# Kernel optimization log

Hardware: AMD Instinct MI355X
Metric: run time of the kernel (lower is better)

The kernel has to match this reference:

```python
import jax, jax.numpy as jnp
import numpy as np

B, C, H, W = 8, 512, 48, 48
DK = C // 8            # query/key dim
L = max(H, W)          # rel_pos_length == H == W
R = 2 * L - 1          # num relative shifts
N = H * W
EPS = 1e-5


def setup_inputs() -> dict:
    key = jax.random.key(0)
    ks = jax.random.split(key, 20)
    d = {
        "x": jax.random.normal(ks[0], (B, C, H, W), jnp.float32),
        "Wq": jax.random.normal(ks[1], (DK, C), jnp.float32) * 0.02,
        "bq": jnp.zeros((DK,), jnp.float32),
        "q_scale": jnp.ones((DK,), jnp.float32),
        "q_bias": jnp.zeros((DK,), jnp.float32),
        "Wk": jax.random.normal(ks[2], (DK, C), jnp.float32) * 0.02,
        "bk": jnp.zeros((DK,), jnp.float32),
        "k_scale": jnp.ones((DK,), jnp.float32),
        "k_bias": jnp.zeros((DK,), jnp.float32),
        "Wv": jax.random.normal(ks[3], (C, C), jnp.float32) * 0.02,
        "bv": jnp.zeros((C,), jnp.float32),
        "v_scale": jnp.ones((C,), jnp.float32),
        "v_bias": jnp.zeros((C,), jnp.float32),
        "rel_rows": jax.random.normal(ks[4], (R, DK), jnp.float32),
        "rel_columns": jax.random.normal(ks[5], (R, DK), jnp.float32),
        "bnr_scale": jnp.ones((C,), jnp.float32),
        "bnr_bias": jnp.zeros((C,), jnp.float32),
        "bnc_scale": jnp.ones((C,), jnp.float32),
        "bnc_bias": jnp.zeros((C,), jnp.float32),
        # gamma is a learned scalar (init 0 in torch; nonzero here so output != x)
        "gamma": jax.random.normal(ks[6], (1,), jnp.float32) * 0.1,
    }
    return d


def _bn(y, scale, bias):
    # train-mode BatchNorm2d: batch stats over (B,H,W), biased variance
    m = jnp.mean(y, axis=(0, 2, 3))
    v = jnp.mean((y - m[None, :, None, None]) ** 2, axis=(0, 2, 3))
    yn = (y - m[None, :, None, None]) * jax.lax.rsqrt(v + EPS)[None, :, None, None]
    return yn * scale[None, :, None, None] + bias[None, :, None, None]


def _conv_bn_relu(x, Wc, bc, scale, bias):
    y = jnp.einsum('bchw,oc->bohw', x, Wc) + bc[None, :, None, None]  # 1x1 conv
    return jax.nn.relu(_bn(y, scale, bias))


def _rel_P(l, rel_table):
    # compute_reindexing_tensor reduces to a one-hot over shift (i - x) since
    # |i-x| <= L always holds when L == l; Ih @ rel_table == gather by shift.
    x = jnp.arange(l)[:, None]
    i = jnp.arange(l)[None, :]
    idx = i - x + (L - 1)                 # (l, l) in [0, 2L-2]
    return rel_table[idx]                 # (l, l, DK)


def reference(x, Wq, bq, q_scale, q_bias, Wk, bk, k_scale, k_bias,
              Wv, bv, v_scale, v_bias, rel_rows, rel_columns,
              bnr_scale, bnr_bias, bnc_scale, bnc_bias, gamma):
    q = _conv_bn_relu(x, Wq, bq, q_scale, q_bias).reshape(B, DK, N)   # proj_query^T
    k = _conv_bn_relu(x, Wk, bk, k_scale, k_bias).reshape(B, DK, N)
    v = _conv_bn_relu(x, Wv, bv, v_scale, v_bias).reshape(B, C, N)

    energy = jnp.einsum('bdn,bdm->bnm', q, k)        # (B,N,N) = Q^T K (unscaled)
    attention = jax.nn.softmax(energy, axis=-1)
    out = jnp.einsum('bcj,bij->bci', v, attention)   # V A^T
    attn_mask = out.reshape(B, C, H, W)

    # relative position terms: Eh = V (Ph Q^T), Ew = V (Pw Q^T)
    Ph = _rel_P(H, rel_rows).reshape(N, DK)          # (N,DK) since H==W
    Mh = jnp.einsum('nd,bdm->bnm', Ph, q)
    Eh = jnp.einsum('bcn,bnm->bcm', v, Mh).reshape(B, C, H, W)
    Eh = _bn(Eh, bnr_scale, bnr_bias)

    Pw = _rel_P(W, rel_columns).reshape(N, DK)
    Mw = jnp.einsum('nd,bdm->bnm', Pw, q)
    Ew = jnp.einsum('bcn,bnm->bcm', v, Mw).reshape(B, C, H, W)
    Ew = _bn(Ew, bnc_scale, bnc_bias)

    attn_mask = attn_mask + Eh + Ew
    return gamma[0] * attn_mask + x
```

## Files before the change

kernel.cpp:

```cpp
#include <hip/hip_runtime.h>
#include <math.h>

#define BB   8
#define CIN  512
#define NSP  2304
#define OCH  640
#define LL   48

typedef __attribute__((ext_vector_type(8))) short bf16x8;
typedef __attribute__((ext_vector_type(8))) unsigned short u16x8;
typedef __attribute__((ext_vector_type(4))) float f32x4;

__device__ inline unsigned short f2bf(float f) {
  unsigned int u = __float_as_uint(f);
  unsigned int r = (u + 0x7fffu + ((u >> 16) & 1u)) >> 16;
  return (unsigned short)r;
}
__device__ inline float bf2f(unsigned short h) {
  return __uint_as_float(((unsigned int)h) << 16);
}


#define STAGE128x64(GP, LD, LDSN)                                              \
  {                                                                            \
    const unsigned short* gsrc_ = (GP);                                        \
    _Pragma("unroll") for (int cc_ = 0; cc_ < 4; cc_++) {                      \
      int base_ = w * 2048 + cc_ * 512;                                        \
      int row_ = w * 32 + cc_ * 8 + rsub;                                      \
      __builtin_amdgcn_global_load_lds(                                        \
          (const __attribute__((address_space(1))) void*)(gsrc_ +              \
              (size_t)row_ * (LD) + scolb),                                    \
          (__attribute__((address_space(3))) void*)&(LDSN)[base_], 16, 0, 0);  \
    }                                                                          \
  }

#define STAGE8(GPA, LDA, LA, GPB, LDB, LB)                                     \
  {                                                                            \
    if (w < 4) {                                                               \
      const unsigned short* gsrc_ = (GPA);                                     \
      _Pragma("unroll") for (int cc_ = 0; cc_ < 4; cc_++) {                    \
        int base_ = w * 2048 + cc_ * 512;                                      \
        int row_ = w * 32 + cc_ * 8 + rsub;                                    \
        __builtin_amdgcn_global_load_lds(                                      \
            (const __attribute__((address_space(1))) void*)(gsrc_ +            \
                (size_t)row_ * (LDA) + scolb),                                 \
            (__attribute__((address_space(3))) void*)&(LA)[base_], 16, 0, 0);  \
      }                                                                        \
    } else {                                                                   \
      const unsigned short* gsrc_ = (GPB);                                     \
      int w2_ = w - 4;                                                         \
      _Pragma("unroll") for (int cc_ = 0; cc_ < 4; cc_++) {                    \
        int base_ = w2_ * 2048 + cc_ * 512;                                    \
        int row_ = w2_ * 32 + cc_ * 8 + rsub;                                  \
        __builtin_amdgcn_global_load_lds(                                      \
            (const __attribute__((address_space(1))) void*)(gsrc_ +            \
                (size_t)row_ * (LDB) + scolb),                                 \
            (__attribute__((address_space(3))) void*)&(LB)[base_], 16, 0, 0);  \
      }                                                                        \
    }                                                                          \
  }

#define MFMA_STEP(APTR, BPTR)                                                  \
  _Pragma("unroll") for (int kk_ = 0; kk_ < 2; kk_++) {                        \
    bf16x8 af_[4], bf_[4];                                                     \
    int kcol_ = (((kk_ * 4 + (lane >> 4)) ^ (lane & 7)) * 8);                  \
    _Pragma("unroll") for (int m_ = 0; m_ < 4; m_++)                           \
      af_[m_] = *(const bf16x8*)&(APTR)[(wr * 64 + m_ * 16 + (lane & 15)) * 64 + kcol_]; \
    _Pragma("unroll") for (int n_ = 0; n_ < 4; n_++)                           \
      bf_[n_] = *(const bf16x8*)&(BPTR)[(wc * 64 + n_ * 16 + (lane & 15)) * 64 + kcol_]; \
    _Pragma("unroll") for (int m_ = 0; m_ < 4; m_++)                           \
      _Pragma("unroll") for (int n_ = 0; n_ < 4; n_++)                         \
        acc[m_][n_] = __builtin_amdgcn_mfma_f32_16x16x32_bf16(                 \
            af_[m_], bf_[n_], acc[m_][n_], 0, 0, 0);                           \
  }

#define MFMA_STEP8(APTR, BPTR)                                                 \
  _Pragma("unroll") for (int kk_ = 0; kk_ < 2; kk_++) {                        \
    bf16x8 af_[4], bf_[2];                                                     \
    int kcol_ = (((kk_ * 4 + (lane >> 4)) ^ (lane & 7)) * 8);                  \
    _Pragma("unroll") for (int m_ = 0; m_ < 4; m_++)                           \
      af_[m_] = *(const bf16x8*)&(APTR)[(wr * 64 + m_ * 16 + (lane & 15)) * 64 + kcol_]; \
    _Pragma("unroll") for (int n_ = 0; n_ < 2; n_++)                           \
      bf_[n_] = *(const bf16x8*)&(BPTR)[(wc * 32 + n_ * 16 + (lane & 15)) * 64 + kcol_]; \
    _Pragma("unroll") for (int m_ = 0; m_ < 4; m_++)                           \
      _Pragma("unroll") for (int n_ = 0; n_ < 2; n_++)                         \
        acc[m_][n_] = __builtin_amdgcn_mfma_f32_16x16x32_bf16(                 \
            af_[m_], bf_[n_], acc[m_][n_], 0, 0, 0);                           \
  }

#define MFMA_PROLOG()                                                          \
  const int tid = threadIdx.x;                                                 \
  const int lane = tid & 63;                                                   \
  const int w = tid >> 6;                                                      \
  const int wr = w >> 1, wc = w & 1;                                           \
  const int rsub = lane >> 3;                                                  \
  const int scolb = ((lane & 7) ^ rsub) * 8;                                   \
  f32x4 acc[4][4] = {};                                                        \
  (void)scolb; (void)rsub; (void)wr; (void)wc;

__global__ __launch_bounds__(256) void prep_all(
    const float* __restrict__ Wq, const float* __restrict__ bq,
    const float* __restrict__ Wk, const float* __restrict__ bk,
    const float* __restrict__ Wv, const float* __restrict__ bv,
    const float* __restrict__ rel_rows, const float* __restrict__ rel_cols,
    unsigned short* __restrict__ Wstb, float* __restrict__ bst,
    unsigned short* __restrict__ Pcatb) {
  int idx = blockIdx.x * 256 + threadIdx.x;
  if (idx < OCH * CIN) {
    int row = idx >> 9;
    float val;
    if (row < 64)       val = Wq[idx];
    else if (row < 128) val = Wk[idx - (64 << 9)];
    else                val = Wv[idx - (128 << 9)];
    Wstb[idx] = f2bf(val);
    if (idx < OCH) {
      float bval;
      if (idx < 64)       bval = bq[idx];
      else if (idx < 128) bval = bk[idx - 64];
      else                bval = bv[idx - 128];
      bst[idx] = bval;
    }
  } else {
    int p = idx - OCH * CIN;
    int dd = p / NSP;
    int n = p - dd * NSP;
    int xr = n / LL;
    int ic = n - xr * LL;
    int shift = ic - xr + (LL - 1);
    float val = (dd < 64) ? rel_rows[shift * 64 + dd]
                          : rel_cols[shift * 64 + (dd - 64)];
    Pcatb[p] = f2bf(val);
  }
}

__global__ __launch_bounds__(256) void transpose_x(
    const float* __restrict__ x, unsigned short* __restrict__ xTb) {
  __shared__ float t[64][65];
  const int n0 = blockIdx.x * 64;
  const int c0 = blockIdx.y * 64;
  const int b = blockIdx.z;
  const int j = threadIdx.x & 63;
  const int g = threadIdx.x >> 6;
  const float* xp = x + (size_t)b * CIN * NSP;
#pragma unroll
  for (int i = 0; i < 16; i++) {
    int cl = g * 16 + i;
    t[cl][j] = xp[(size_t)(c0 + cl) * NSP + n0 + j];
  }
  __syncthreads();
  unsigned short* op = xTb + (size_t)b * NSP * CIN;
#pragma unroll
  for (int i = 0; i < 16; i++) {
    int nl = g * 16 + i;
    op[(size_t)(n0 + nl) * CIN + c0 + j] = f2bf(t[j][nl]);
  }
}

__global__ __launch_bounds__(256) void proj_mfma(
    const unsigned short* __restrict__ Wstb, const float* __restrict__ bst,
    const unsigned short* __restrict__ xTb, unsigned short* __restrict__ y16,
    float* __restrict__ part1, float* __restrict__ part2) {
  __shared__ unsigned short As[2][8192];
  __shared__ unsigned short Bs[2][8192];
  int sw = ((blockIdx.x & 7) * 90) + (blockIdx.x >> 3);
  const int rb = sw % 5;
  const int nb = (sw / 5) % 18;
  const int b = sw / 90;
  const int r0 = rb * 128;
  const int n0 = nb * 128;
  MFMA_PROLOG();
  const unsigned short* A = Wstb + (size_t)r0 * CIN;
  const unsigned short* B = xTb + (size_t)b * NSP * CIN + (size_t)n0 * CIN;

  STAGE128x64(A, CIN, As[0]);
  STAGE128x64(B, CIN, Bs[0]);
  asm volatile("s_waitcnt vmcnt(0)" ::: "memory");
  __builtin_amdgcn_sched_barrier(0);
  __builtin_amdgcn_s_barrier();

  int cur = 0;
  for (int t = 0; t < 8; ++t) {
    if (t + 1 < 8) {
      STAGE128x64(A + (t + 1) * 64, CIN, As[cur ^ 1]);
      STAGE128x64(B + (t + 1) * 64, CIN, Bs[cur ^ 1]);
    }
    __builtin_amdgcn_s_setprio(1);
    MFMA_STEP(As[cur], Bs[cur]);
    __builtin_amdgcn_s_setprio(0);
    asm volatile("s_waitcnt vmcnt(0)" ::: "memory");
    __builtin_amdgcn_sched_barrier(0);
    __builtin_amdgcn_s_barrier();
    cur ^= 1;
  }

  float* sp = (float*)&As[0][0];
#pragma unroll
  for (int m = 0; m < 4; m++) {
#pragma unroll
    for (int r = 0; r < 4; r++) {
      int rl = wr * 64 + m * 16 + (lane >> 4) * 4 + r;
      int row = r0 + rl;
      float bias = bst[row];
      float s1 = 0.f, s2 = 0.f;
#pragma unroll
      for (int n = 0; n < 4; n++) {
        float yv = acc[m][n][r] + bias;
        s1 += yv;
        s2 += yv * yv;
        y16[((size_t)b * OCH + row) * NSP + n0 + wc * 64 + n * 16 + (lane & 15)] = f2bf(yv);
      }
#pragma unroll
      for (int off = 1; off < 16; off <<= 1) {
        s1 += __shfl_xor(s1, off);
        s2 += __shfl_xor(s2, off);
      }
      if ((lane & 15) == 0) {
        sp[rl * 2 + wc] = s1;
        sp[256 + rl * 2 + wc] = s2;
      }
    }
  }
  __syncthreads();
  if (tid < 128) {
    size_t pbase = ((size_t)b * 18 + nb) * OCH + r0 + tid;
    part1[pbase] = sp[tid * 2] + sp[tid * 2 + 1];
    part2[pbase] = sp[256 + tid * 2] + sp[256 + tid * 2 + 1];
  }
}

__global__ __launch_bounds__(256) void bn_finalize(
    const float* __restrict__ part1, const float* __restrict__ part2,
    const float* __restrict__ qs_, const float* __restrict__ qb_,
    const float* __restrict__ ks_, const float* __restrict__ kb_,
    const float* __restrict__ vs_, const float* __restrict__ vb_,
    float* __restrict__ chanA, float* __restrict__ chanB) {
  const int ch = blockIdx.x;
  const int tid = threadIdx.x;
  float s1 = 0.f, s2 = 0.f;
  for (int t = tid; t < 144; t += 256) {
    s1 += part1[(size_t)t * OCH + ch];
    s2 += part2[(size_t)t * OCH + ch];
  }
  __shared__ float sb[8];
#pragma unroll
  for (int off = 32; off > 0; off >>= 1) {
    s1 += __shfl_down(s1, off);
    s2 += __shfl_down(s2, off);
  }
  int lane = tid & 63, wid = tid >> 6;
  if (lane == 0) { sb[wid] = s1; sb[4 + wid] = s2; }
  __syncthreads();
  if (tid == 0) {
    float ts  = sb[0] + sb[1] + sb[2] + sb[3];
    float ts2 = sb[4] + sb[5] + sb[6] + sb[7];
    const float inv = 1.f / (float)(BB * NSP);
    float mean = ts * inv;
    float var  = ts2 * inv - mean * mean;
    float scale, bias;
    if (ch < 64)       { scale = qs_[ch];       bias = qb_[ch]; }
    else if (ch < 128) { scale = ks_[ch - 64];  bias = kb_[ch - 64]; }
    else               { scale = vs_[ch - 128]; bias = vb_[ch - 128]; }
    float a = scale * rsqrtf(var + 1e-5f);
    chanA[ch] = a;
    chanB[ch] = bias - mean * a;
  }
}

__global__ __launch_bounds__(256) void bn_post(
    unsigned short* __restrict__ y16, const float* __restrict__ chanA,
    const float* __restrict__ chanB, unsigned short* __restrict__ qTb,
    unsigned short* __restrict__ kTb) {
  __shared__ unsigned short qk[128][64];
  const int n0 = blockIdx.x * 64;
  const int b = blockIdx.y;
  const int tid = threadIdx.x;
#pragma unroll
  for (int k = 0; k < 20; k++) {
    int v = tid + k * 256;
    int ch = v >> 3;
    int n8 = (v & 7) * 8;
    size_t off = ((size_t)b * OCH + ch) * NSP + n0 + n8;
    float a = chanA[ch], bo = chanB[ch];
    ushort4 u0 = *(ushort4*)&y16[off];
    ushort4 u1 = *(ushort4*)&y16[off + 4];
    ushort4 o0, o1;
    o0.x = f2bf(fmaxf(0.f, a * bf2f(u0.x) + bo));
    o0.y = f2bf(fmaxf(0.f, a * bf2f(u0.y) + bo));
    o0.z = f2bf(fmaxf(0.f, a * bf2f(u0.z) + bo));
    o0.w = f2bf(fmaxf(0.f, a * bf2f(u0.w) + bo));
    o1.x = f2bf(fmaxf(0.f, a * bf2f(u1.x) + bo));
    o1.y = f2bf(fmaxf(0.f, a * bf2f(u1.y) + bo));
    o1.z = f2bf(fmaxf(0.f, a * bf2f(u1.z) + bo));
    o1.w = f2bf(fmaxf(0.f, a * bf2f(u1.w) + bo));
    *(ushort4*)&y16[off] = o0;
    *(ushort4*)&y16[off + 4] = o1;
    if (ch < 128) {
      *(ushort4*)&qk[ch][n8] = o0;
      *(ushort4*)&qk[ch][n8 + 4] = o1;
    }
  }
  __syncthreads();
#pragma unroll
  for (int it = 0; it < 4; it++) {
    int combo = (tid >> 6) + it * 4;
    int plane = combo >> 3;
    int dg = combo & 7;
    int nl = tid & 63;
    unsigned short tmp[8];
#pragma unroll
    for (int d = 0; d < 8; d++) tmp[d] = qk[plane * 64 + dg * 8 + d][nl];
    unsigned short* out = (plane == 0) ? qTb : kTb;
    *(u16x8*)&out[((size_t)b * NSP + n0 + nl) * 64 + dg * 8] = *(u16x8*)tmp;
  }
}

__global__ __launch_bounds__(256) void qsum_kernel(
    const unsigned short* __restrict__ y16, float* __restrict__ qs) {
  int bd = blockIdx.x;
  int b = bd >> 6, d = bd & 63;
  const ushort4* p = (const ushort4*)(y16 + ((size_t)b * OCH + d) * NSP);
  float s = 0.f;
  for (int t = threadIdx.x; t < NSP / 4; t += 256) {
    ushort4 u = p[t];
    s += bf2f(u.x) + bf2f(u.y) + bf2f(u.z) + bf2f(u.w);
  }
  __shared__ float sb[4];
#pragma unroll
  for (int off = 32; off > 0; off >>= 1) s += __shfl_down(s, off);
  int lane = threadIdx.x & 63, wid = threadIdx.x >> 6;
  if (lane == 0) sb[wid] = s;
  __syncthreads();
  if (threadIdx.x == 0) qs[bd] = sb[0] + sb[1] + sb[2] + sb[3];
}

__global__ __launch_bounds__(256) void gq_mfma(
    const unsigned short* __restrict__ y16, float* __restrict__ Gqp) {
  __shared__ float wlds[4 * 4096];
  const int bx = blockIdx.x;
  const int b = bx >> 2, kc = bx & 3;
  const int tid = threadIdx.x;
  const int lane = tid & 63;
  const int w = tid >> 6;
  const unsigned short* q = y16 + (size_t)b * OCH * NSP;
  f32x4 acc[4][4] = {};
  for (int k0 = kc * 576 + w * 32; k0 < (kc + 1) * 576; k0 += 128) {
    bf16x8 fr[4];
#pragma unroll
    for (int f = 0; f < 4; f++) {
      int row = f * 16 + (lane & 15);
      fr[f] = *(const bf16x8*)&q[(size_t)row * NSP + k0 + (lane >> 4) * 8];
    }
#pragma unroll
    for (int fm = 0; fm < 4; fm++)
#pragma unroll
      for (int fn = 0; fn < 4; fn++)
        acc[fm][fn] = __builtin_amdgcn_mfma_f32_16x16x32_bf16(
            fr[fm], fr[fn], acc[fm][fn], 0, 0, 0);
  }
#pragma unroll
  for (int fm = 0; fm < 4; fm++)
#pragma unroll
    for (int fn = 0; fn < 4; fn++)
#pragma unroll
      for (int r = 0; r < 4; r++) {
        int d = fm * 16 + (lane >> 4) * 4 + r;
        int e = fn * 16 + (lane & 15);
        wlds[w * 4096 + d * 64 + e] = acc[fm][fn][r];
      }
  __syncthreads();
  for (int t = tid; t < 4096; t += 256)
    Gqp[(size_t)bx * 4096 + t] =
        wlds[t] + wlds[4096 + t] + wlds[8192 + t] + wlds[12288 + t];
}

__global__ __launch_bounds__(256) void energy_mfma(
    const unsigned short* __restrict__ qTb, const unsigned short* __restrict__ kTb,
    unsigned short* __restrict__ Pp, float* __restrict__ Ppart) {
  __shared__ unsigned short As[8192];
  __shared__ unsigned short Bs[8192];
  int sw = ((blockIdx.x & 7) * 324) + (blockIdx.x >> 3);
  const int jb = sw % 18;
  const int ib = (sw / 18) % 18;
  const int b = sw / 324;
  const int i0 = ib * 128;
  const int j0 = jb * 128;
  MFMA_PROLOG();
  STAGE128x64(qTb + ((size_t)b * NSP + i0) * 64, 64, As);
  STAGE128x64(kTb + ((size_t)b * NSP + j0) * 64, 64, Bs);
  __syncthreads();
  MFMA_STEP(As, Bs);
  __syncthreads();
  float* sp = (float*)As;
  unsigned short* pp = Pp + (size_t)b * NSP * NSP;
#pragma unroll
  for (int m = 0; m < 4; m++) {
#pragma unroll
    for (int r = 0; r < 4; r++) {
      int rl = wr * 64 + m * 16 + (lane >> 4) * 4 + r;
      int i = i0 + rl;
      float s1 = 0.f;
#pragma unroll
      for (int n = 0; n < 4; n++) {
        int j = j0 + wc * 64 + n * 16 + (lane & 15);
        unsigned short h = f2bf(__expf(acc[m][n][r]));
        pp[(size_t)i * NSP + j] = h;
        s1 += bf2f(h);
      }
#pragma unroll
      for (int off = 1; off < 16; off <<= 1) s1 += __shfl_xor(s1, off);
      if ((lane & 15) == 0) sp[rl * 2 + wc] = s1;
    }
  }
  __syncthreads();
  if (tid < 128)
    Ppart[((size_t)b * 18 + jb) * NSP + i0 + tid] = sp[tid * 2] + sp[tid * 2 + 1];
}

__global__ __launch_bounds__(256) void up_mfma(
    const unsigned short* __restrict__ y16, const unsigned short* __restrict__ Pcatb,
    float* __restrict__ Upart) {
  __shared__ unsigned short As[2][8192];
  __shared__ unsigned short Bs[2][8192];
  int sw = ((blockIdx.x & 7) * 24) + (blockIdx.x >> 3);
  const int cb = sw % 4;
  const int kc = (sw / 4) % 6;
  const int b = sw / 24;
  const int c0 = cb * 128;
  MFMA_PROLOG();
  const unsigned short* A = y16 + ((size_t)b * OCH + 128 + c0) * NSP + kc * 384;
  const unsigned short* B = Pcatb + kc * 384;

  STAGE128x64(A, NSP, As[0]);
  STAGE128x64(B, NSP, Bs[0]);
  asm volatile("s_waitcnt vmcnt(0)" ::: "memory");
  __builtin_amdgcn_sched_barrier(0);
  __builtin_amdgcn_s_barrier();

  int cur = 0;
  for (int t = 0; t < 6; ++t) {
    if (t + 1 < 6) {
      STAGE128x64(A + (t + 1) * 64, NSP, As[cur ^ 1]);
      STAGE128x64(B + (t + 1) * 64, NSP, Bs[cur ^ 1]);
    }
    __builtin_amdgcn_s_setprio(1);
    MFMA_STEP(As[cur], Bs[cur]);
    __builtin_amdgcn_s_setprio(0);
    asm volatile("s_waitcnt vmcnt(0)" ::: "memory");
    __builtin_amdgcn_sched_barrier(0);
    __builtin_amdgcn_s_barrier();
    cur ^= 1;
  }

  float* up = Upart + ((size_t)kc * BB + b) * CIN * 128 + (size_t)c0 * 128;
#pragma unroll
  for (int m = 0; m < 4; m++)
#pragma unroll
    for (int r = 0; r < 4; r++) {
      int rl = wr * 64 + m * 16 + (lane >> 4) * 4 + r;
#pragma unroll
      for (int n = 0; n < 4; n++) {
        int col = wc * 64 + n * 16 + (lane & 15);
        up[(size_t)rl * 128 + col] = acc[m][n][r];
      }
    }
}

__global__ __launch_bounds__(256) void rel_finalize(
    const float* __restrict__ Upart, const float* __restrict__ Gqp,
    const float* __restrict__ qs,
    const float* __restrict__ bnr_s, const float* __restrict__ bnr_b,
    const float* __restrict__ bnc_s, const float* __restrict__ bnc_b,
    float* __restrict__ offc, unsigned short* __restrict__ Ucb) {
  const int c = blockIdx.x;
  const int tid = threadIdx.x;
  __shared__ float U[8][128];
  __shared__ float ghw[2];
  for (int t = tid; t < 1024; t += 256) {
    int b = t >> 7, dd = t & 127;
    float s = 0.f;
#pragma unroll
    for (int kc = 0; kc < 6; kc++)
      s += Upart[(((size_t)kc * BB + b) * CIN + c) * 128 + dd];
    U[b][dd] = s;
  }
  __syncthreads();
  if (tid < 64) {
    const int d = tid;
    float s1h = 0.f, s2h = 0.f, s1w = 0.f, s2w = 0.f;
    for (int b = 0; b < BB; b++) {
      float uh = U[b][d], uw = U[b][64 + d];
      float th = 0.f, tw = 0.f;
#pragma unroll
      for (int kc = 0; kc < 4; kc++) {
        const float* G = Gqp + ((size_t)(b * 4 + kc)) * 4096 + d * 64;
        for (int e = 0; e < 64; e++) {
          float g = G[e];
          th += g * U[b][e];
          tw += g * U[b][64 + e];
        }
      }
      float qsd = qs[b * 64 + d];
      s1h += uh * qsd;
      s2h += uh * th;
      s1w += uw * qsd;
      s2w += uw * tw;
    }
#pragma unroll
    for (int off = 32; off > 0; off >>= 1) {
      s1h += __shfl_down(s1h, off);
      s2h += __shfl_down(s2h, off);
      s1w += __shfl_down(s1w, off);
      s2w += __shfl_down(s2w, off);
    }
    if (d == 0) {
      const float inv = 1.f / (float)(BB * NSP);
      float mh = s1h * inv, vh = s2h * inv - mh * mh;
      float mw = s1w * inv, vw = s2w * inv - mw * mw;
      float gch = bnr_s[c] * rsqrtf(vh + 1e-5f);
      float gcw = bnc_s[c] * rsqrtf(vw + 1e-5f);
      ghw[0] = gch;
      ghw[1] = gcw;
      offc[c] = (bnr_b[c] - mh * gch) + (bnc_b[c] - mw * gcw);
    }
  }
  __syncthreads();
  for (int t = tid; t < 512; t += 256) {
    int b = t >> 6, d = t & 63;
    Ucb[((size_t)b * CIN + c) * 64 + d] =
        f2bf(U[b][d] * ghw[0] + U[b][64 + d] * ghw[1]);
  }
}

__global__ __launch_bounds__(512) void attn_fused_gemm(
    const unsigned short* __restrict__ y16,
    const unsigned short* __restrict__ Pp,
    const float* __restrict__ Ppart,
    const unsigned short* __restrict__ Ucb,
    const unsigned short* __restrict__ qTb,
    const float* __restrict__ offc,
    const float* __restrict__ gammap,
    const float* __restrict__ x,
    float* __restrict__ dst) {
  __shared__ unsigned short As[2][8192];
  __shared__ unsigned short Bs[2][8192];
  __shared__ float rzl[128];
  int sw = ((blockIdx.x & 7) * 72) + (blockIdx.x >> 3);
  const int cb = sw % 4;
  const int ib = (sw / 4) % 18;
  const int b = sw / 72;
  const int c0 = cb * 128;
  const int i0 = ib * 128;
  const int tid = threadIdx.x;
  const int lane = tid & 63;
  const int w = tid >> 6;
  const int wr = w >> 2, wc = w & 3;
  const int rsub = lane >> 3;
  const int scolb = ((lane & 7) ^ rsub) * 8;
  f32x4 acc[4][2] = {};

  const unsigned short* A = y16 + ((size_t)b * OCH + 128 + c0) * NSP;
  const unsigned short* B = Pp + (size_t)b * NSP * NSP + (size_t)i0 * NSP;
  const unsigned short* A2 = Ucb + (size_t)b * CIN * 64 + (size_t)c0 * 64;
  const unsigned short* B2 = qTb + (size_t)b * NSP * 64 + (size_t)i0 * 64;

  STAGE8(A, NSP, As[0], B, NSP, Bs[0]);
  if (tid < 128) {
    float s = 0.f;
#pragma unroll
    for (int jb = 0; jb < 18; jb++)
      s += Ppart[((size_t)b * 18 + jb) * NSP + i0 + tid];
    rzl[tid] = 1.f / s;
  }
  asm volatile("s_waitcnt vmcnt(0)" ::: "memory");
  __builtin_amdgcn_sched_barrier(0);
  __builtin_amdgcn_s_barrier();

  int cur = 0;
  for (int tt = 0; tt < 37; ++tt) {
    if (tt + 1 < 36) {
      STAGE8(A + (tt + 1) * 64, NSP, As[cur ^ 1], B + (tt + 1) * 64, NSP, Bs[cur ^ 1]);
    } else if (tt + 1 == 36) {
      STAGE8(A2, 64, As[cur ^ 1], B2, 64, Bs[cur ^ 1]);
    }
    if (tt == 36) {
#pragma unroll
      for (int n = 0; n < 2; n++) {
        float rz = rzl[wc * 32 + n * 16 + (lane & 15)];
#pragma unroll
        for (int m = 0; m < 4; m++)
#pragma unroll
          for (int r = 0; r < 4; r++) acc[m][n][r] *= rz;
      }
    }
    __builtin_amdgcn_s_setprio(1);
    MFMA_STEP8(As[cur], Bs[cur]);
    __builtin_amdgcn_s_setprio(0);
    asm volatile("s_waitcnt vmcnt(0)" ::: "memory");
    __builtin_amdgcn_sched_barrier(0);
    __builtin_amdgcn_s_barrier();
    cur ^= 1;
  }

  const float gmm = gammap[0];
  const float* xp = x + (size_t)b * CIN * NSP;
  float* dp = dst + (size_t)b * CIN * NSP;
#pragma unroll
  for (int m = 0; m < 4; m++) {
#pragma unroll
    for (int r = 0; r < 4; r++) {
      int c = c0 + wr * 64 + m * 16 + (lane >> 4) * 4 + r;
      float off = offc[c];
#pragma unroll
      for (int n = 0; n < 2; n++) {
        int i = i0 + wc * 32 + n * 16 + (lane & 15);
        size_t o = (size_t)c * NSP + i;
        dp[o] = gmm * (acc[m][n][r] + off) + xp[o];
      }
    }
  }
}

extern "C" void kernel_launch(void* const* d_in, const int* in_sizes, int n_in,
                              void* d_out, int out_size, void* d_ws, size_t ws_size,
                              hipStream_t stream) {
  const float* x        = (const float*)d_in[0];
  const float* Wq       = (const float*)d_in[1];
  const float* bq       = (const float*)d_in[2];
  const float* q_scale  = (const float*)d_in[3];
  const float* q_bias   = (const float*)d_in[4];
  const float* Wk       = (const float*)d_in[5];
  const float* bk       = (const float*)d_in[6];
  const float* k_scale  = (const float*)d_in[7];
  const float* k_bias   = (const float*)d_in[8];
  const float* Wv       = (const float*)d_in[9];
  const float* bv       = (const float*)d_in[10];
  const float* v_scale  = (const float*)d_in[11];
  const float* v_bias   = (const float*)d_in[12];
  const float* rel_rows = (const float*)d_in[13];
  const float* rel_cols = (const float*)d_in[14];
  const float* bnr_s    = (const float*)d_in[15];
  const float* bnr_b    = (const float*)d_in[16];
  const float* bnc_s    = (const float*)d_in[17];
  const float* bnc_b    = (const float*)d_in[18];
  const float* gamma    = (const float*)d_in[19];
  float* dst = (float*)d_out;

  float* ws = (float*)d_ws;
  size_t o = 0;
  unsigned short* Wstb = (unsigned short*)(ws + o); o += (size_t)OCH * CIN / 2;
  float* bst    = ws + o; o += 1024;
  float* chanA  = ws + o; o += 1024;
  float* chanB  = ws + o; o += 1024;
  unsigned short* Pcatb = (unsigned short*)(ws + o); o += (size_t)128 * NSP / 2;
  unsigned short* y16 = (unsigned short*)(ws + o); o += (size_t)BB * OCH * NSP / 2;
  unsigned short* xTb = (unsigned short*)(ws + o); o += (size_t)BB * NSP * CIN / 2;
  unsigned short* Pp  = (unsigned short*)(ws + o); o += (size_t)BB * NSP * NSP / 2;
  float* Ppart  = ws + o; o += (size_t)BB * 18 * NSP;
  float* Upart  = ws + o; o += (size_t)6 * BB * CIN * 128;
  float* Gqp    = ws + o; o += (size_t)32 * 4096;
  float* part1  = ws + o; o += (size_t)BB * 18 * OCH;
  float* part2  = ws + o; o += (size_t)BB * 18 * OCH;
  float* qs     = ws + o; o += 1024;
  float* offc   = ws + o; o += 1024;
  unsigned short* qTb = (unsigned short*)(ws + o); o += (size_t)BB * NSP * 64 / 2;
  unsigned short* kTb = (unsigned short*)(ws + o); o += (size_t)BB * NSP * 64 / 2;
  unsigned short* Ucb = (unsigned short*)(ws + o); o += (size_t)BB * CIN * 64 / 2;

  prep_all<<<(OCH * CIN + 128 * NSP) / 256, 256, 0, stream>>>(
      Wq, bq, Wk, bk, Wv, bv, rel_rows, rel_cols, Wstb, bst, Pcatb);
  transpose_x<<<dim3(NSP / 64, CIN / 64, BB), 256, 0, stream>>>(x, xTb);

  proj_mfma<<<720, 256, 0, stream>>>(Wstb, bst, xTb, y16, part1, part2);
  bn_finalize<<<OCH, 256, 0, stream>>>(part1, part2, q_scale, q_bias, k_scale,
                                       k_bias, v_scale, v_bias, chanA, chanB);
  bn_post<<<dim3(36, BB), 256, 0, stream>>>(y16, chanA, chanB, qTb, kTb);
  qsum_kernel<<<BB * 64, 256, 0, stream>>>(y16, qs);
  gq_mfma<<<32, 256, 0, stream>>>(y16, Gqp);

  energy_mfma<<<2592, 256, 0, stream>>>(qTb, kTb, Pp, Ppart);

  up_mfma<<<192, 256, 0, stream>>>(y16, Pcatb, Upart);
  rel_finalize<<<CIN, 256, 0, stream>>>(Upart, Gqp, qs, bnr_s, bnr_b,
                                        bnc_s, bnc_b, offc, Ucb);

  attn_fused_gemm<<<576, 512, 0, stream>>>(y16, Pp, Ppart, Ucb, qTb, offc, gamma, x, dst);
}
```

Measured before the change: 240.2 us.

## Deepen attention GEMM pipeline, coalesce energy stores, fold qsum into gq kernel

The attention GEMM moves from double to quad-buffered LDS staging with a prefetch distance of two and partial vmcnt waits, so global loads overlap more MFMA work. The energy kernel now stages its exp tile in LDS and writes it out as 16-byte vectors instead of scattered 2-byte stores. The separate qsum kernel is removed and its row sums are computed as per-chunk partials inside gq_mfma, then summed in rel_finalize. Doubling LDS in the attention kernel (about 128 KB) may reduce occupancy.

```diff
diff --git a/kernel.cpp b/kernel.cpp
--- a/kernel.cpp
+++ b/kernel.cpp
@@ -6,6 +6,9 @@
 #define NSP  2304
 #define OCH  640
 #define LL   48
+
+#define AS1 __attribute__((address_space(1)))
+#define AS3 __attribute__((address_space(3)))
 
 typedef __attribute__((ext_vector_type(8))) short bf16x8;
 typedef __attribute__((ext_vector_type(8))) unsigned short u16x8;
@@ -28,9 +31,8 @@
       int base_ = w * 2048 + cc_ * 512;                                        \
       int row_ = w * 32 + cc_ * 8 + rsub;                                      \
       __builtin_amdgcn_global_load_lds(                                        \
-          (const __attribute__((address_space(1))) void*)(gsrc_ +              \
-              (size_t)row_ * (LD) + scolb),                                    \
-          (__attribute__((address_space(3))) void*)&(LDSN)[base_], 16, 0, 0);  \
+          (const AS1 void*)(gsrc_ + (size_t)row_ * (LD) + scolb),              \
+          (AS3 void*)&(LDSN)[base_], 16, 0, 0);                                \
     }                                                                          \
   }
 
@@ -42,9 +44,8 @@
         int base_ = w * 2048 + cc_ * 512;                                      \
         int row_ = w * 32 + cc_ * 8 + rsub;                                    \
         __builtin_amdgcn_global_load_lds(                                      \
-            (const __attribute__((address_space(1))) void*)(gsrc_ +            \
-                (size_t)row_ * (LDA) + scolb),                                 \
-            (__attribute__((address_space(3))) void*)&(LA)[base_], 16, 0, 0);  \
+            (const AS1 void*)(gsrc_ + (size_t)row_ * (LDA) + scolb),           \
+            (AS3 void*)&(LA)[base_], 16, 0, 0);                                \
       }                                                                        \
     } else {                                                                   \
       const unsigned short* gsrc_ = (GPB);                                     \
@@ -53,9 +54,8 @@
         int base_ = w2_ * 2048 + cc_ * 512;                                    \
         int row_ = w2_ * 32 + cc_ * 8 + rsub;                                  \
         __builtin_amdgcn_global_load_lds(                                      \
-            (const __attribute__((address_space(1))) void*)(gsrc_ +            \
-                (size_t)row_ * (LDB) + scolb),                                 \
-            (__attribute__((address_space(3))) void*)&(LB)[base_], 16, 0, 0);  \
+            (const AS1 void*)(gsrc_ + (size_t)row_ * (LDB) + scolb),           \
+            (AS3 void*)&(LB)[base_], 16, 0, 0);                                \
       }                                                                        \
     }                                                                          \
   }
@@ -314,27 +314,9 @@
   }
 }
 
-__global__ __launch_bounds__(256) void qsum_kernel(
-    const unsigned short* __restrict__ y16, float* __restrict__ qs) {
-  int bd = blockIdx.x;
-  int b = bd >> 6, d = bd & 63;
-  const ushort4* p = (const ushort4*)(y16 + ((size_t)b * OCH + d) * NSP);
-  float s = 0.f;
-  for (int t = threadIdx.x; t < NSP / 4; t += 256) {
-    ushort4 u = p[t];
-    s += bf2f(u.x) + bf2f(u.y) + bf2f(u.z) + bf2f(u.w);
-  }
-  __shared__ float sb[4];
-#pragma unroll
-  for (int off = 32; off > 0; off >>= 1) s += __shfl_down(s, off);
-  int lane = threadIdx.x & 63, wid = threadIdx.x >> 6;
-  if (lane == 0) sb[wid] = s;
-  __syncthreads();
-  if (threadIdx.x == 0) qs[bd] = sb[0] + sb[1] + sb[2] + sb[3];
-}
-
 __global__ __launch_bounds__(256) void gq_mfma(
-    const unsigned short* __restrict__ y16, float* __restrict__ Gqp) {
+    const unsigned short* __restrict__ y16, float* __restrict__ Gqp,
+    float* __restrict__ qsp) {
   __shared__ float wlds[4 * 4096];
   const int bx = blockIdx.x;
   const int b = bx >> 2, kc = bx & 3;
@@ -367,6 +349,17 @@
         int e = fn * 16 + (lane & 15);
         wlds[w * 4096 + d * 64 + e] = acc[fm][fn][r];
       }
+  {
+    float s = 0.f;
+    const unsigned short* qrow = q + (size_t)(tid >> 2) * NSP + kc * 576 + (tid & 3) * 144;
+    for (int i = 0; i < 144; i += 4) {
+      ushort4 u = *(const ushort4*)&qrow[i];
+      s += bf2f(u.x) + bf2f(u.y) + bf2f(u.z) + bf2f(u.w);
+    }
+    s += __shfl_down(s, 1);
+    s += __shfl_down(s, 2);
+    if ((tid & 3) == 0) qsp[bx * 64 + (tid >> 2)] = s;
+  }
   __syncthreads();
   for (int t = tid; t < 4096; t += 256)
     Gqp[(size_t)bx * 4096 + t] =
@@ -376,8 +369,8 @@
 __global__ __launch_bounds__(256) void energy_mfma(
     const unsigned short* __restrict__ qTb, const unsigned short* __restrict__ kTb,
     unsigned short* __restrict__ Pp, float* __restrict__ Ppart) {
-  __shared__ unsigned short As[8192];
-  __shared__ unsigned short Bs[8192];
+  __shared__ unsigned short lds[16384];
+  __shared__ float rs[256];
   int sw = ((blockIdx.x & 7) * 324) + (blockIdx.x >> 3);
   const int jb = sw % 18;
   const int ib = (sw / 18) % 18;
@@ -385,35 +378,39 @@
   const int i0 = ib * 128;
   const int j0 = jb * 128;
   MFMA_PROLOG();
-  STAGE128x64(qTb + ((size_t)b * NSP + i0) * 64, 64, As);
-  STAGE128x64(kTb + ((size_t)b * NSP + j0) * 64, 64, Bs);
-  __syncthreads();
-  MFMA_STEP(As, Bs);
-  __syncthreads();
-  float* sp = (float*)As;
-  unsigned short* pp = Pp + (size_t)b * NSP * NSP;
+  STAGE128x64(qTb + ((size_t)b * NSP + i0) * 64, 64, lds);
+  STAGE128x64(kTb + ((size_t)b * NSP + j0) * 64, 64, (lds + 8192));
+  __syncthreads();
+  MFMA_STEP(lds, (lds + 8192));
+  __syncthreads();
 #pragma unroll
   for (int m = 0; m < 4; m++) {
 #pragma unroll
     for (int r = 0; r < 4; r++) {
       int rl = wr * 64 + m * 16 + (lane >> 4) * 4 + r;
-      int i = i0 + rl;
       float s1 = 0.f;
 #pragma unroll
       for (int n = 0; n < 4; n++) {
-        int j = j0 + wc * 64 + n * 16 + (lane & 15);
         unsigned short h = f2bf(__expf(acc[m][n][r]));
-        pp[(size_t)i * NSP + j] = h;
+        lds[rl * 128 + wc * 64 + n * 16 + (lane & 15)] = h;
         s1 += bf2f(h);
       }
 #pragma unroll
       for (int off = 1; off < 16; off <<= 1) s1 += __shfl_xor(s1, off);
-      if ((lane & 15) == 0) sp[rl * 2 + wc] = s1;
-    }
-  }
-  __syncthreads();
+      if ((lane & 15) == 0) rs[rl * 2 + wc] = s1;
+    }
+  }
+  __syncthreads();
+  unsigned short* pp = Pp + (size_t)b * NSP * NSP;
+#pragma unroll
+  for (int c8 = tid; c8 < 2048; c8 += 256) {
+    int il = c8 >> 4;
+    int jl = (c8 & 15) * 8;
+    u16x8 v = *(const u16x8*)&lds[il * 128 + jl];
+    *(u16x8*)&pp[(size_t)(i0 + il) * NSP + j0 + jl] = v;
+  }
   if (tid < 128)
-    Ppart[((size_t)b * 18 + jb) * NSP + i0 + tid] = sp[tid * 2] + sp[tid * 2 + 1];
+    Ppart[((size_t)b * 18 + jb) * NSP + i0 + tid] = rs[tid * 2] + rs[tid * 2 + 1];
 }
 
 __global__ __launch_bounds__(256) void up_mfma(
@@ -467,7 +464,7 @@
 
 __global__ __launch_bounds__(256) void rel_finalize(
     const float* __restrict__ Upart, const float* __restrict__ Gqp,
-    const float* __restrict__ qs,
+    const float* __restrict__ qsp,
     const float* __restrict__ bnr_s, const float* __restrict__ bnr_b,
     const float* __restrict__ bnc_s, const float* __restrict__ bnc_b,
     float* __restrict__ offc, unsigned short* __restrict__ Ucb) {
@@ -490,6 +487,7 @@
     for (int b = 0; b < BB; b++) {
       float uh = U[b][d], uw = U[b][64 + d];
       float th = 0.f, tw = 0.f;
+      float qsd = 0.f;
 #pragma unroll
       for (int kc = 0; kc < 4; kc++) {
         const float* G = Gqp + ((size_t)(b * 4 + kc)) * 4096 + d * 64;
@@ -498,8 +496,8 @@
           th += g * U[b][e];
           tw += g * U[b][64 + e];
         }
-      }
-      float qsd = qs[b * 64 + d];
+        qsd += qsp[(b * 4 + kc) * 64 + d];
+      }
       s1h += uh * qsd;
       s2h += uh * th;
       s1w += uw * qsd;
@@ -541,8 +539,8 @@
     const float* __restrict__ gammap,
     const float* __restrict__ x,
     float* __restrict__ dst) {
-  __shared__ unsigned short As[2][8192];
-  __shared__ unsigned short Bs[2][8192];
+  __shared__ unsigned short As[4][8192];
+  __shared__ unsigned short Bs[4][8192];
   __shared__ float rzl[128];
   int sw = ((blockIdx.x & 7) * 72) + (blockIdx.x >> 3);
   const int cb = sw % 4;
@@ -556,14 +554,14 @@
   const int wr = w >> 2, wc = w & 3;
   const int rsub = lane >> 3;
   const int scolb = ((lane & 7) ^ rsub) * 8;
+  const int l15 = lane & 15, l4 = lane >> 4;
   f32x4 acc[4][2] = {};
 
   const unsigned short* A = y16 + ((size_t)b * OCH + 128 + c0) * NSP;
   const unsigned short* B = Pp + (size_t)b * NSP * NSP + (size_t)i0 * NSP;
   const unsigned short* A2 = Ucb + (size_t)b * CIN * 64 + (size_t)c0 * 64;
-  const unsigned short* B2 = qTb + (size_t)b * NSP * 64 + (size_t)i0 * 64;
-
-  STAGE8(A, NSP, As[0], B, NSP, Bs[0]);
+  const unsigned short* B2 = qTb + ((size_t)b * NSP + i0) * 64;
+
   if (tid < 128) {
     float s = 0.f;
 #pragma unroll
@@ -571,34 +569,39 @@
       s += Ppart[((size_t)b * 18 + jb) * NSP + i0 + tid];
     rzl[tid] = 1.f / s;
   }
-  asm volatile("s_waitcnt vmcnt(0)" ::: "memory");
+  asm volatile("s_waitcnt lgkmcnt(0)" ::: "memory");
   __builtin_amdgcn_sched_barrier(0);
-  __builtin_amdgcn_s_barrier();
-
-  int cur = 0;
-  for (int tt = 0; tt < 37; ++tt) {
-    if (tt + 1 < 36) {
-      STAGE8(A + (tt + 1) * 64, NSP, As[cur ^ 1], B + (tt + 1) * 64, NSP, Bs[cur ^ 1]);
-    } else if (tt + 1 == 36) {
-      STAGE8(A2, 64, As[cur ^ 1], B2, 64, Bs[cur ^ 1]);
-    }
-    if (tt == 36) {
-#pragma unroll
-      for (int n = 0; n < 2; n++) {
-        float rz = rzl[wc * 32 + n * 16 + (lane & 15)];
-#pragma unroll
-        for (int m = 0; m < 4; m++)
-#pragma unroll
-          for (int r = 0; r < 4; r++) acc[m][n][r] *= rz;
-      }
-    }
-    __builtin_amdgcn_s_setprio(1);
-    MFMA_STEP8(As[cur], Bs[cur]);
-    __builtin_amdgcn_s_setprio(0);
-    asm volatile("s_waitcnt vmcnt(0)" ::: "memory");
+
+  STAGE8(A, NSP, As[0], B, NSP, Bs[0]);
+  STAGE8(A + 64, NSP, As[1], B + 64, NSP, Bs[1]);
+
+  for (int t = 0; t < 37; ++t) {
+    if (t + 2 < 36) {
+      STAGE8(A + (t + 2) * 64, NSP, As[(t + 2) & 3], B + (t + 2) * 64, NSP, Bs[(t + 2) & 3]);
+      asm volatile("s_waitcnt vmcnt(8)" ::: "memory");
+    } else if (t + 2 == 36) {
+      STAGE8(A2, 64, As[(t + 2) & 3], B2, 64, Bs[(t + 2) & 3]);
+      asm volatile("s_waitcnt vmcnt(8)" ::: "memory");
+    } else if (t + 1 <= 36) {
+      asm volatile("s_waitcnt vmcnt(4)" ::: "memory");
+    } else {
+      asm volatile("s_waitcnt vmcnt(0)" ::: "memory");
+    }
     __builtin_amdgcn_sched_barrier(0);
     __builtin_amdgcn_s_barrier();
-    cur ^= 1;
+    if (t == 36) {
+#pragma unroll
+      for (int n = 0; n < 2; n++) {
+        float rz = rzl[wc * 32 + n * 16 + l15];
+#pragma unroll
+        for (int m = 0; m < 4; m++)
+#pragma unroll
+          for (int r = 0; r < 4; r++) acc[m][n][r] *= rz;
+      }
+    }
+    __builtin_amdgcn_s_setprio(1);
+    MFMA_STEP8(As[t & 3], Bs[t & 3]);
+    __builtin_amdgcn_s_setprio(0);
   }
 
   const float gmm = gammap[0];
@@ -608,11 +611,11 @@
   for (int m = 0; m < 4; m++) {
 #pragma unroll
     for (int r = 0; r < 4; r++) {
-      int c = c0 + wr * 64 + m * 16 + (lane >> 4) * 4 + r;
+      int c = c0 + wr * 64 + m * 16 + l4 * 4 + r;
       float off = offc[c];
 #pragma unroll
       for (int n = 0; n < 2; n++) {
-        int i = i0 + wc * 32 + n * 16 + (lane & 15);
+        int i = i0 + wc * 32 + n * 16 + l15;
         size_t o = (size_t)c * NSP + i;
         dp[o] = gmm * (acc[m][n][r] + off) + xp[o];
       }
@@ -660,7 +663,7 @@
   float* Gqp    = ws + o; o += (size_t)32 * 4096;
   float* part1  = ws + o; o += (size_t)BB * 18 * OCH;
   float* part2  = ws + o; o += (size_t)BB * 18 * OCH;
-  float* qs     = ws + o; o += 1024;
+  float* qsp    = ws + o; o += (size_t)32 * 64;
   float* offc   = ws + o; o += 1024;
   unsigned short* qTb = (unsigned short*)(ws + o); o += (size_t)BB * NSP * 64 / 2;
   unsigned short* kTb = (unsigned short*)(ws + o); o += (size_t)BB * NSP * 64 / 2;
@@ -674,14 +677,14 @@
   bn_finalize<<<OCH, 256, 0, stream>>>(part1, part2, q_scale, q_bias, k_scale,
                                        k_bias, v_scale, v_bias, chanA, chanB);
   bn_post<<<dim3(36, BB), 256, 0, stream>>>(y16, chanA, chanB, qTb, kTb);
-  qsum_kernel<<<BB * 64, 256, 0, stream>>>(y16, qs);
-  gq_mfma<<<32, 256, 0, stream>>>(y16, Gqp);
+  gq_mfma<<<32, 256, 0, stream>>>(y16, Gqp, qsp);
 
   energy_mfma<<<2592, 256, 0, stream>>>(qTb, kTb, Pp, Ppart);
 
   up_mfma<<<192, 256, 0, stream>>>(y16, Pcatb, Upart);
-  rel_finalize<<<CIN, 256, 0, stream>>>(Upart, Gqp, qs, bnr_s, bnr_b,
+  rel_finalize<<<CIN, 256, 0, stream>>>(Upart, Gqp, qsp, bnr_s, bnr_b,
                                         bnc_s, bnc_b, offc, Ucb);
 
-  attn_fused_gemm<<<576, 512, 0, stream>>>(y16, Pp, Ppart, Ucb, qTb, offc, gamma, x, dst);
-}
+  attn_fused_gemm<<<576, 512, 0, stream>>>(y16, Pp, Ppart, Ucb, qTb, offc,
+                                           gamma, x, dst);
+}
```

Measured after the change: 245.0 us. No clear change (+2.0%).
